# Kernel optimization log

Measured on AMD Instinct MI355X. Metric: run time of the kernel, lower is better.

The kernel has to match this reference:

```python
import jax, jax.numpy as jnp
import numpy as np

BF16_MIN = -3.3895313892515355e+38  # torch.finfo(torch.bfloat16).min
B, S, D = 2, 2048, 2048
H, KVH = 32, 8
HD = D // H  # 64


def setup_inputs() -> dict:
    key = jax.random.key(0)
    ks = jax.random.split(key, 7)
    scale = 0.02
    x = jax.random.normal(ks[0], (B, S, D), dtype=jnp.float32)
    # rotary tables as in llama2.c: theta = 10000^{-2i/hd}
    inv_freq = 1.0 / (10000.0 ** (np.arange(0, HD, 2, dtype=np.float32) / HD))
    t = np.arange(S, dtype=np.float32)
    freqs = np.outer(t, inv_freq)  # (S, HD//2)
    freqs_cos = jnp.asarray(np.cos(freqs))
    freqs_sin = jnp.asarray(np.sin(freqs))
    wq = jax.random.normal(ks[1], (H * HD, D), dtype=jnp.float32) * scale
    wk = jax.random.normal(ks[2], (KVH * HD, D), dtype=jnp.float32) * scale
    wv = jax.random.normal(ks[3], (KVH * HD, D), dtype=jnp.float32) * scale
    wo = jax.random.normal(ks[4], (D, H * HD), dtype=jnp.float32) * scale
    attn_mask = jnp.ones((B, S), dtype=jnp.int32)
    return {"x": x, "freqs_cos": freqs_cos, "freqs_sin": freqs_sin,
            "wq": wq, "wk": wk, "wv": wv, "wo": wo, "attn_mask": attn_mask}


def _rope(x, cos, sin):
    # x: (b, s, h, hd) -> split into interleaved real/imag pairs
    b, s, h, hd = x.shape
    xr = x[..., 0::2]
    xi = x[..., 1::2]
    cos = cos[None, :, None, :]  # (1, s, 1, hd//2)
    sin = sin[None, :, None, :]
    out_r = xr * cos - xi * sin
    out_i = xr * sin + xi * cos
    return jnp.stack([out_r, out_i], axis=-1).reshape(b, s, h, hd)


def reference(x, freqs_cos, freqs_sin, wq, wk, wv, wo, attn_mask):
    b, s, d = x.shape
    n_rep = H // KVH
    xq = jnp.einsum('bsd,ed->bse', x, wq).reshape(b, s, H, HD)
    xk = jnp.einsum('bsd,ed->bse', x, wk).reshape(b, s, KVH, HD)
    xv = jnp.einsum('bsd,ed->bse', x, wv).reshape(b, s, KVH, HD)
    xq = _rope(xq, freqs_cos, freqs_sin)
    xk = _rope(xk, freqs_cos, freqs_sin)
    # GQA repeat_kv: (b, s, kvh, hd) -> (b, s, kvh*n_rep, hd)
    xk = jnp.repeat(xk, n_rep, axis=2)
    xv = jnp.repeat(xv, n_rep, axis=2)
    # (b, h, s, hd)
    xq = xq.transpose(0, 2, 1, 3)
    xk = xk.transpose(0, 2, 1, 3)
    xv = xv.transpose(0, 2, 1, 3)
    causal = jnp.triu(jnp.full((s, s), BF16_MIN, dtype=x.dtype), k=1)[None, None]
    pad = jnp.where(attn_mask[:, None, :] == 0, BF16_MIN, 0.0).astype(x.dtype)  # (b,1,s) -> broadcast over query
    combined = causal + pad[:, None, :, :]  # (b,1,s,s)
    scores = jnp.einsum('bhqd,bhkd->bhqk', xq, xk) / np.sqrt(HD).astype(x.dtype)
    scores = jax.nn.softmax(scores + combined, axis=-1)
    out = jnp.einsum('bhqk,bhkd->bhqd', scores, xv)
    out = out.transpose(0, 2, 1, 3).reshape(b, s, H * HD)
    return jnp.einsum('bse,de->bsd', out, wo)
```

## Files before the change

### kernel.cpp

```cpp
#include <hip/hip_runtime.h>

typedef unsigned short u16;
typedef unsigned int u32;
typedef __attribute__((ext_vector_type(8))) short bf16x8;
typedef __attribute__((ext_vector_type(4))) float f32x4;

#define S_LEN 2048
#define QKV_N 3072
#define CEXP 0.18033688011f
#define M32C 5.77078016f

__device__ __forceinline__ u16 f2bf(float f) {
  u32 u = __builtin_bit_cast(u32, f);
  u32 r = (u + 0x7FFFu + ((u >> 16) & 1u)) >> 16;
  return (u16)r;
}
__device__ __forceinline__ u32 cvtpk(float lo, float hi) {
  u32 r;
  asm("v_cvt_pk_bf16_f32 %0, %1, %2" : "=v"(r) : "v"(lo), "v"(hi));
  return r;
}
__device__ __forceinline__ void gload16(const void* g, void* l) {
  __builtin_amdgcn_global_load_lds(
      (const __attribute__((address_space(1))) u32*)g,
      (__attribute__((address_space(3))) u32*)l, 16, 0, 0);
}

__global__ void cast_all(const float* __restrict__ x, const float* __restrict__ wq,
                         const float* __restrict__ wk, const float* __restrict__ wv,
                         const float* __restrict__ wo, u16* __restrict__ xb,
                         u16* __restrict__ wqkvb, u16* __restrict__ wob) {
  int i = blockIdx.x * 256 + threadIdx.x;
  const float* s;
  u16* d;
  int so, dofs;
  if (i < 2097152) {
    s = x; d = xb; so = i; dofs = i;
  } else if (i < 3145728) {
    s = wq; d = wqkvb; so = i - 2097152; dofs = so;
  } else if (i < 3407872) {
    s = wk; d = wqkvb; so = i - 3145728; dofs = so + 1048576;
  } else if (i < 3670016) {
    s = wv; d = wqkvb; so = i - 3407872; dofs = so + 1310720;
  } else {
    s = wo; d = wob; so = i - 3670016; dofs = so;
  }
  float4 v = ((const float4*)s)[so];
  ((uint2*)d)[dofs] = make_uint2(cvtpk(v.x, v.y), cvtpk(v.z, v.w));
}

template <int BM, int BN, int WM, int WN, int OUT_BF16, int ROPE>
__global__ __launch_bounds__(512, 2) void gemm_bt2(const u16* __restrict__ A,
                                                   const u16* __restrict__ B,
                                                   void* __restrict__ Cv,
                                                   int K, int ldc, int nbx,
                                                   const float* __restrict__ fc,
                                                   const float* __restrict__ fs,
                                                   u16* __restrict__ vt) {
  constexpr int MR = BM / WM / 16;
  constexpr int NR = BN / WN / 16;
  constexpr int MR2 = MR / 2, NR2 = NR / 2;
  constexpr int AR = BM / 64, BR = BN / 64;
  __shared__ u16 As0[BM * 64], As1[BM * 64];
  __shared__ u16 Bs0[BN * 64], Bs1[BN * 64];

  const int tid = threadIdx.x;
  const int lane = tid & 63, w = tid >> 6;
  const int wm = w / WN, wn = w % WN;
  const int g = lane >> 4, r16 = lane & 15;
  const int swz = r16 & 7;

  const int nwg = gridDim.x;
  const int q = nwg >> 3, r = nwg & 7;
  const int xcd = blockIdx.x & 7, off = blockIdx.x >> 3;
  const int wg = (xcd < r ? xcd * (q + 1) : r * (q + 1) + (xcd - r) * q) + off;
  const int m0 = (wg / nbx) * BM, n0 = (wg % nbx) * BN;

  const int rowi = tid >> 3;
  const int scol = ((tid & 7) ^ (rowi & 7)) * 8;
  const u16* Ag0 = A + (size_t)(m0 + rowi) * K + scol;
  const u16* Bg0 = B + (size_t)(n0 + rowi) * K + scol;

  f32x4 acc[MR][NR];
#pragma unroll
  for (int mi = 0; mi < MR; ++mi)
#pragma unroll
    for (int ni = 0; ni < NR; ++ni) acc[mi][ni] = f32x4{0.f, 0.f, 0.f, 0.f};

  auto stage = [&](int kb, u16* Ad, u16* Bd) {
#pragma unroll
    for (int rr = 0; rr < AR; ++rr)
      gload16(Ag0 + (size_t)rr * 64 * K + kb, Ad + rr * 4096 + tid * 8);
#pragma unroll
    for (int rr = 0; rr < BR; ++rr)
      gload16(Bg0 + (size_t)rr * 64 * K + kb, Bd + rr * 4096 + tid * 8);
  };

  auto compute = [&](const u16* Asrc, const u16* Bsrc) {
    bf16x8 ac[MR2][2], bc[NR][2];
    const u16* Aw = Asrc + (wm * MR * 16 + r16) * 64;
    const u16* Bw = Bsrc + (wn * NR * 16 + r16) * 64;
#pragma unroll
    for (int mi = 0; mi < MR2; ++mi)
#pragma unroll
      for (int kk = 0; kk < 2; ++kk)
        ac[mi][kk] = *(const bf16x8*)(Aw + mi * 1024 + ((kk * 4 + g) ^ swz) * 8);
#pragma unroll
    for (int ni = 0; ni < NR2; ++ni)
#pragma unroll
      for (int kk = 0; kk < 2; ++kk)
        bc[ni][kk] = *(const bf16x8*)(Bw + ni * 1024 + ((kk * 4 + g) ^ swz) * 8);
    __builtin_amdgcn_s_setprio(1);
#pragma unroll
    for (int mi = 0; mi < MR2; ++mi)
#pragma unroll
      for (int ni = 0; ni < NR2; ++ni)
#pragma unroll
        for (int kk = 0; kk < 2; ++kk)
          acc[mi][ni] = __builtin_amdgcn_mfma_f32_16x16x32_bf16(
              ac[mi][kk], bc[ni][kk], acc[mi][ni], 0, 0, 0);
    __builtin_amdgcn_s_setprio(0);
#pragma unroll
    for (int ni = NR2; ni < NR; ++ni)
#pragma unroll
      for (int kk = 0; kk < 2; ++kk)
        bc[ni][kk] = *(const bf16x8*)(Bw + ni * 1024 + ((kk * 4 + g) ^ swz) * 8);
    __builtin_amdgcn_s_setprio(1);
#pragma unroll
    for (int mi = 0; mi < MR2; ++mi)
#pragma unroll
      for (int ni = NR2; ni < NR; ++ni)
#pragma unroll
        for (int kk = 0; kk < 2; ++kk)
          acc[mi][ni] = __builtin_amdgcn_mfma_f32_16x16x32_bf16(
              ac[mi][kk], bc[ni][kk], acc[mi][ni], 0, 0, 0);
    __builtin_amdgcn_s_setprio(0);
#pragma unroll
    for (int mi = 0; mi < MR2; ++mi)
#pragma unroll
      for (int kk = 0; kk < 2; ++kk)
        ac[mi][kk] =
            *(const bf16x8*)(Aw + (MR2 + mi) * 1024 + ((kk * 4 + g) ^ swz) * 8);
    __builtin_amdgcn_s_setprio(1);
#pragma unroll
    for (int mi = 0; mi < MR2; ++mi)
#pragma unroll
      for (int ni = NR2; ni < NR; ++ni)
#pragma unroll
        for (int kk = 0; kk < 2; ++kk)
          acc[MR2 + mi][ni] = __builtin_amdgcn_mfma_f32_16x16x32_bf16(
              ac[mi][kk], bc[ni][kk], acc[MR2 + mi][ni], 0, 0, 0);
    __builtin_amdgcn_s_setprio(0);
    __builtin_amdgcn_s_setprio(1);
#pragma unroll
    for (int mi = 0; mi < MR2; ++mi)
#pragma unroll
      for (int ni = 0; ni < NR2; ++ni)
#pragma unroll
        for (int kk = 0; kk < 2; ++kk)
          acc[MR2 + mi][ni] = __builtin_amdgcn_mfma_f32_16x16x32_bf16(
              ac[mi][kk], bc[ni][kk], acc[MR2 + mi][ni], 0, 0, 0);
    __builtin_amdgcn_s_setprio(0);
  };

  const int NT = K >> 6;
  stage(0, As0, Bs0);
  __syncthreads();
  for (int t = 0; t < NT; t += 2) {
    if (t + 1 < NT) stage((t + 1) * 64, As1, Bs1);
    compute(As0, Bs0);
    __syncthreads();
    if (t + 2 < NT) stage((t + 2) * 64, As0, Bs0);
    compute(As1, Bs1);
    __syncthreads();
  }

  if (ROPE && n0 >= 2560) {
#pragma unroll
    for (int mi = 0; mi < MR; ++mi)
#pragma unroll
      for (int ni = 0; ni < NR; ++ni) {
        int row = m0 + wm * MR * 16 + mi * 16 + g * 4;
        int col = n0 + wn * NR * 16 + ni * 16 + r16;
        int kv = (col - 2560) >> 6;
        int d = (col - 2560) & 63;
        int b_ = row >> 11, s0 = row & 2047;
        *(uint2*)&vt[(size_t)((b_ * 8 + kv) * 64 + d) * 2048 + s0] =
            make_uint2(cvtpk(acc[mi][ni][0], acc[mi][ni][1]),
                       cvtpk(acc[mi][ni][2], acc[mi][ni][3]));
      }
    return;
  }

#pragma unroll
  for (int mi = 0; mi < MR; ++mi)
#pragma unroll
    for (int ni = 0; ni < NR; ++ni) {
      int row = m0 + wm * MR * 16 + mi * 16 + g * 4;
      int col = n0 + wn * NR * 16 + ni * 16 + r16;
#pragma unroll
      for (int j = 0; j < 4; ++j) {
        float v = acc[mi][ni][j];
        if (ROPE) {
          float pv = __shfl_xor(v, 1);
          int s = (row + j) & (S_LEN - 1);
          int fi = (col >> 1) & 31;
          float c = fc[s * 32 + fi], sn = fs[s * 32 + fi];
          v = fmaf(pv, (r16 & 1) ? sn : -sn, v * c);
        }
        if (OUT_BF16)
          ((u16*)Cv)[(size_t)(row + j) * ldc + col] = f2bf(v);
        else
          ((float*)Cv)[(size_t)(row + j) * ldc + col] = v;
      }
    }
}

__global__ __launch_bounds__(256, 3) void attn_fwd(const u16* __restrict__ qkv,
                                                   const u16* __restrict__ vt,
                                                   u16* __restrict__ aout) {
  __shared__ u16 Ks[2][64 * 64];
  __shared__ u16 Vs[2][64 * 64];
  __shared__ u16 Ps[4][16 * 64];

  const int bh = blockIdx.x;
  const int y = blockIdx.y;
  const int qt = (y < 4) ? (15 - y) : (y < 8) ? (y - 4) : (y < 12) ? y : (19 - y);
  const int b = bh >> 5, h = bh & 31, kvh = h >> 2;
  const int tid = threadIdx.x;
  const int w = tid >> 6, lane = tid & 63;
  const int g = lane >> 4, r16 = lane & 15;
  const int q0w = qt * 128 + w * 32;

  const u16* kbase = qkv + (size_t)b * S_LEN * QKV_N + 2048 + kvh * 64;
  const u16* vbase = vt + (size_t)(b * 8 + kvh) * 64 * S_LEN;

  const int srow = lane >> 3;
  const int scol = ((lane & 7) * 8) ^ (srow * 8);
  const int swz = (r16 & 7) * 8;

  bf16x8 qf[2][2];
#pragma unroll
  for (int qs = 0; qs < 2; ++qs) {
    const u16* qrow =
        qkv + (size_t)(b * S_LEN + q0w + qs * 16 + r16) * QKV_N + h * 64;
#pragma unroll
    for (int dh = 0; dh < 2; ++dh)
      qf[qs][dh] = *(const bf16x8*)(qrow + dh * 32 + g * 8);
  }

  f32x4 oacc[2][4];
#pragma unroll
  for (int qs = 0; qs < 2; ++qs)
#pragma unroll
    for (int dt = 0; dt < 4; ++dt) oacc[qs][dt] = f32x4{0.f, 0.f, 0.f, 0.f};
  float lsum[2] = {0.f, 0.f};

  const int nt = qt * 2 + 2;
  const int ntw = ((q0w + 31) >> 6) + 1;

#pragma unroll
  for (int c2 = 0; c2 < 2; ++c2) {
    int c = w * 2 + c2;
    gload16(kbase + (size_t)(c * 8 + srow) * QKV_N + scol, &Ks[0][c * 512]);
    gload16(vbase + (size_t)(c * 8 + srow) * 2048 + scol, &Vs[0][c * 512]);
  }
  __syncthreads();

  int cur = 0;
  for (int t = 0; t < nt; ++t) {
    if (t + 1 < nt) {
      int kk0 = (t + 1) * 64;
#pragma unroll
      for (int c2 = 0; c2 < 2; ++c2) {
        int c = w * 2 + c2;
        gload16(kbase + (size_t)(kk0 + c * 8 + srow) * QKV_N + scol,
                &Ks[cur ^ 1][c * 512]);
        gload16(vbase + (size_t)(c * 8 + srow) * 2048 + kk0 + scol,
                &Vs[cur ^ 1][c * 512]);
      }
    }
    if (t < ntw) {
      const int k0 = t * 64;
      bf16x8 kf[4][2];
#pragma unroll
      for (int ks = 0; ks < 4; ++ks)
#pragma unroll
        for (int dh = 0; dh < 2; ++dh)
          kf[ks][dh] = *(const bf16x8*)&Ks[cur][(ks * 16 + r16) * 64 +
                                               ((dh * 32 + g * 8) ^ swz)];
      bf16x8 vfc[2][4];
#pragma unroll
      for (int ks2 = 0; ks2 < 2; ++ks2)
#pragma unroll
        for (int dt = 0; dt < 4; ++dt)
          vfc[ks2][dt] = *(const bf16x8*)&Vs[cur][(dt * 16 + r16) * 64 +
                                                  ((ks2 * 32 + g * 8) ^ swz)];
      const bool needmask = (k0 + 63 > q0w);
#pragma unroll
      for (int qs = 0; qs < 2; ++qs) {
        f32x4 st[4];
        __builtin_amdgcn_s_setprio(1);
#pragma unroll
        for (int ks = 0; ks < 4; ++ks) {
          f32x4 a = f32x4{0.f, 0.f, 0.f, 0.f};
          a = __builtin_amdgcn_mfma_f32_16x16x32_bf16(kf[ks][0], qf[qs][0], a, 0, 0, 0);
          a = __builtin_amdgcn_mfma_f32_16x16x32_bf16(kf[ks][1], qf[qs][1], a, 0, 0, 0);
          st[ks] = a;
        }
        __builtin_amdgcn_s_setprio(0);
        const int qg = q0w + qs * 16 + r16;
        if (needmask) {
#pragma unroll
          for (int ks = 0; ks < 4; ++ks)
#pragma unroll
            for (int j = 0; j < 4; ++j)
              if (k0 + ks * 16 + g * 4 + j > qg) st[ks][j] = -__builtin_inff();
        }
        float ps = 0.f;
#pragma unroll
        for (int ks = 0; ks < 4; ++ks) {
          float p0 = exp2f(fmaf(st[ks][0], CEXP, -M32C));
          float p1 = exp2f(fmaf(st[ks][1], CEXP, -M32C));
          float p2 = exp2f(fmaf(st[ks][2], CEXP, -M32C));
          float p3 = exp2f(fmaf(st[ks][3], CEXP, -M32C));
          ps += (p0 + p1) + (p2 + p3);
          *(uint2*)&Ps[w][r16 * 64 + ((ks * 16 + g * 4) ^ swz)] =
              make_uint2(cvtpk(p0, p1), cvtpk(p2, p3));
        }
        lsum[qs] += ps;
        __builtin_amdgcn_s_setprio(1);
#pragma unroll
        for (int ks2 = 0; ks2 < 2; ++ks2) {
          bf16x8 pf =
              *(const bf16x8*)&Ps[w][r16 * 64 + ((ks2 * 32 + g * 8) ^ swz)];
#pragma unroll
          for (int dt = 0; dt < 4; ++dt)
            oacc[qs][dt] = __builtin_amdgcn_mfma_f32_16x16x32_bf16(
                pf, vfc[ks2][dt], oacc[qs][dt], 0, 0, 0);
        }
        __builtin_amdgcn_s_setprio(0);
      }
    }
    __syncthreads();
    cur ^= 1;
  }

#pragma unroll
  for (int qs = 0; qs < 2; ++qs) {
    float l = lsum[qs];
    l += __shfl_xor(l, 16);
    l += __shfl_xor(l, 32);
    float inv = 1.f / l;
    float iv[4];
#pragma unroll
    for (int j = 0; j < 4; ++j) iv[j] = __shfl(inv, g * 4 + j);
#pragma unroll
    for (int dt = 0; dt < 4; ++dt)
#pragma unroll
      for (int j = 0; j < 4; ++j) {
        size_t o = (size_t)(b * S_LEN + q0w + qs * 16 + g * 4 + j) * 2048 +
                   h * 64 + dt * 16 + r16;
        aout[o] = f2bf(oacc[qs][dt][j] * iv[j]);
      }
  }
}

extern "C" void kernel_launch(void* const* d_in, const int* in_sizes, int n_in,
                              void* d_out, int out_size, void* d_ws,
                              size_t ws_size, hipStream_t stream) {
  const float* x = (const float*)d_in[0];
  const float* fc = (const float*)d_in[1];
  const float* fs = (const float*)d_in[2];
  const float* wq = (const float*)d_in[3];
  const float* wk = (const float*)d_in[4];
  const float* wv = (const float*)d_in[5];
  const float* wo = (const float*)d_in[6];
  float* out = (float*)d_out;

  char* ws = (char*)d_ws;
  u16* xb = (u16*)(ws);
  u16* wqkvb = (u16*)(ws + 16777216);
  u16* wob = (u16*)(ws + 29360128);
  u16* qkvb = (u16*)(ws + 37748736);
  u16* vtb = (u16*)(ws + 62914560);
  u16* aoutb = (u16*)(ws + 67108864);

  cast_all<<<18432, 256, 0, stream>>>(x, wq, wk, wv, wo, xb, wqkvb, wob);

  gemm_bt2<128, 128, 2, 4, 1, 1><<<768, 512, 0, stream>>>(
      xb, wqkvb, qkvb, 2048, 3072, 24, fc, fs, vtb);
  attn_fwd<<<dim3(64, 16), 256, 0, stream>>>(qkvb, vtb, aoutb);
  gemm_bt2<128, 128, 2, 4, 0, 0><<<512, 512, 0, stream>>>(
      aoutb, wob, out, 2048, 2048, 16, nullptr, nullptr, nullptr);
}
```

Before: 171.0 us.

## Halve attention query tile to 64 rows, doubling grid and simplifying masking

Each attention block now handles 64 query rows (16 per wave) instead of 128, and the grid doubles to 32 query tiles per head, launched heaviest-first. The per-wave skip of fully masked KV tiles is gone, and masking is applied only on the last (diagonal) tile. This aims for better load balance and occupancy through more, smaller blocks with fewer registers. The cost is that K/V tiles are loaded from global memory twice as often relative to the query work.

```diff
diff --git a/kernel.cpp b/kernel.cpp
--- a/kernel.cpp
+++ b/kernel.cpp
@@ -224,13 +224,12 @@
   __shared__ u16 Ps[4][16 * 64];
 
   const int bh = blockIdx.x;
-  const int y = blockIdx.y;
-  const int qt = (y < 4) ? (15 - y) : (y < 8) ? (y - 4) : (y < 12) ? y : (19 - y);
+  const int qt = 31 - (int)blockIdx.y;
   const int b = bh >> 5, h = bh & 31, kvh = h >> 2;
   const int tid = threadIdx.x;
   const int w = tid >> 6, lane = tid & 63;
   const int g = lane >> 4, r16 = lane & 15;
-  const int q0w = qt * 128 + w * 32;
+  const int q0w = qt * 64 + w * 16;
 
   const u16* kbase = qkv + (size_t)b * S_LEN * QKV_N + 2048 + kvh * 64;
   const u16* vbase = vt + (size_t)(b * 8 + kvh) * 64 * S_LEN;
@@ -239,25 +238,20 @@
   const int scol = ((lane & 7) * 8) ^ (srow * 8);
   const int swz = (r16 & 7) * 8;
 
-  bf16x8 qf[2][2];
-#pragma unroll
-  for (int qs = 0; qs < 2; ++qs) {
-    const u16* qrow =
-        qkv + (size_t)(b * S_LEN + q0w + qs * 16 + r16) * QKV_N + h * 64;
+  bf16x8 qf[2];
+  {
+    const u16* qrow = qkv + (size_t)(b * S_LEN + q0w + r16) * QKV_N + h * 64;
 #pragma unroll
     for (int dh = 0; dh < 2; ++dh)
-      qf[qs][dh] = *(const bf16x8*)(qrow + dh * 32 + g * 8);
-  }
-
-  f32x4 oacc[2][4];
-#pragma unroll
-  for (int qs = 0; qs < 2; ++qs)
-#pragma unroll
-    for (int dt = 0; dt < 4; ++dt) oacc[qs][dt] = f32x4{0.f, 0.f, 0.f, 0.f};
-  float lsum[2] = {0.f, 0.f};
-
-  const int nt = qt * 2 + 2;
-  const int ntw = ((q0w + 31) >> 6) + 1;
+      qf[dh] = *(const bf16x8*)(qrow + dh * 32 + g * 8);
+  }
+
+  f32x4 oacc[4];
+#pragma unroll
+  for (int dt = 0; dt < 4; ++dt) oacc[dt] = f32x4{0.f, 0.f, 0.f, 0.f};
+  float lsum = 0.f;
+
+  const int nt = qt + 1;
 
 #pragma unroll
   for (int c2 = 0; c2 < 2; ++c2) {
@@ -280,7 +274,7 @@
                 &Vs[cur ^ 1][c * 512]);
       }
     }
-    if (t < ntw) {
+    {
       const int k0 = t * 64;
       bf16x8 kf[4][2];
 #pragma unroll
@@ -296,74 +290,66 @@
         for (int dt = 0; dt < 4; ++dt)
           vfc[ks2][dt] = *(const bf16x8*)&Vs[cur][(dt * 16 + r16) * 64 +
                                                   ((ks2 * 32 + g * 8) ^ swz)];
-      const bool needmask = (k0 + 63 > q0w);
-#pragma unroll
-      for (int qs = 0; qs < 2; ++qs) {
-        f32x4 st[4];
-        __builtin_amdgcn_s_setprio(1);
-#pragma unroll
-        for (int ks = 0; ks < 4; ++ks) {
-          f32x4 a = f32x4{0.f, 0.f, 0.f, 0.f};
-          a = __builtin_amdgcn_mfma_f32_16x16x32_bf16(kf[ks][0], qf[qs][0], a, 0, 0, 0);
-          a = __builtin_amdgcn_mfma_f32_16x16x32_bf16(kf[ks][1], qf[qs][1], a, 0, 0, 0);
-          st[ks] = a;
-        }
-        __builtin_amdgcn_s_setprio(0);
-        const int qg = q0w + qs * 16 + r16;
-        if (needmask) {
-#pragma unroll
-          for (int ks = 0; ks < 4; ++ks)
-#pragma unroll
-            for (int j = 0; j < 4; ++j)
-              if (k0 + ks * 16 + g * 4 + j > qg) st[ks][j] = -__builtin_inff();
-        }
-        float ps = 0.f;
-#pragma unroll
-        for (int ks = 0; ks < 4; ++ks) {
-          float p0 = exp2f(fmaf(st[ks][0], CEXP, -M32C));
-          float p1 = exp2f(fmaf(st[ks][1], CEXP, -M32C));
-          float p2 = exp2f(fmaf(st[ks][2], CEXP, -M32C));
-          float p3 = exp2f(fmaf(st[ks][3], CEXP, -M32C));
-          ps += (p0 + p1) + (p2 + p3);
-          *(uint2*)&Ps[w][r16 * 64 + ((ks * 16 + g * 4) ^ swz)] =
-              make_uint2(cvtpk(p0, p1), cvtpk(p2, p3));
-        }
-        lsum[qs] += ps;
-        __builtin_amdgcn_s_setprio(1);
-#pragma unroll
-        for (int ks2 = 0; ks2 < 2; ++ks2) {
-          bf16x8 pf =
-              *(const bf16x8*)&Ps[w][r16 * 64 + ((ks2 * 32 + g * 8) ^ swz)];
-#pragma unroll
-          for (int dt = 0; dt < 4; ++dt)
-            oacc[qs][dt] = __builtin_amdgcn_mfma_f32_16x16x32_bf16(
-                pf, vfc[ks2][dt], oacc[qs][dt], 0, 0, 0);
-        }
-        __builtin_amdgcn_s_setprio(0);
-      }
+      f32x4 st[4];
+      __builtin_amdgcn_s_setprio(1);
+#pragma unroll
+      for (int ks = 0; ks < 4; ++ks) {
+        f32x4 a = f32x4{0.f, 0.f, 0.f, 0.f};
+        a = __builtin_amdgcn_mfma_f32_16x16x32_bf16(kf[ks][0], qf[0], a, 0, 0, 0);
+        a = __builtin_amdgcn_mfma_f32_16x16x32_bf16(kf[ks][1], qf[1], a, 0, 0, 0);
+        st[ks] = a;
+      }
+      __builtin_amdgcn_s_setprio(0);
+      if (t == nt - 1) {
+        const int qg = q0w + r16;
+#pragma unroll
+        for (int ks = 0; ks < 4; ++ks)
+#pragma unroll
+          for (int j = 0; j < 4; ++j)
+            if (k0 + ks * 16 + g * 4 + j > qg) st[ks][j] = -__builtin_inff();
+      }
+      float ps = 0.f;
+#pragma unroll
+      for (int ks = 0; ks < 4; ++ks) {
+        float p0 = exp2f(fmaf(st[ks][0], CEXP, -M32C));
+        float p1 = exp2f(fmaf(st[ks][1], CEXP, -M32C));
+        float p2 = exp2f(fmaf(st[ks][2], CEXP, -M32C));
+        float p3 = exp2f(fmaf(st[ks][3], CEXP, -M32C));
+        ps += (p0 + p1) + (p2 + p3);
+        *(uint2*)&Ps[w][r16 * 64 + ((ks * 16 + g * 4) ^ swz)] =
+            make_uint2(cvtpk(p0, p1), cvtpk(p2, p3));
+      }
+      lsum += ps;
+      __builtin_amdgcn_s_setprio(1);
+#pragma unroll
+      for (int ks2 = 0; ks2 < 2; ++ks2) {
+        bf16x8 pf = *(const bf16x8*)&Ps[w][r16 * 64 + ((ks2 * 32 + g * 8) ^ swz)];
+#pragma unroll
+        for (int dt = 0; dt < 4; ++dt)
+          oacc[dt] = __builtin_amdgcn_mfma_f32_16x16x32_bf16(
+              pf, vfc[ks2][dt], oacc[dt], 0, 0, 0);
+      }
+      __builtin_amdgcn_s_setprio(0);
     }
     __syncthreads();
     cur ^= 1;
   }
 
-#pragma unroll
-  for (int qs = 0; qs < 2; ++qs) {
-    float l = lsum[qs];
-    l += __shfl_xor(l, 16);
-    l += __shfl_xor(l, 32);
-    float inv = 1.f / l;
-    float iv[4];
-#pragma unroll
-    for (int j = 0; j < 4; ++j) iv[j] = __shfl(inv, g * 4 + j);
-#pragma unroll
-    for (int dt = 0; dt < 4; ++dt)
-#pragma unroll
-      for (int j = 0; j < 4; ++j) {
-        size_t o = (size_t)(b * S_LEN + q0w + qs * 16 + g * 4 + j) * 2048 +
-                   h * 64 + dt * 16 + r16;
-        aout[o] = f2bf(oacc[qs][dt][j] * iv[j]);
-      }
-  }
+  float l = lsum;
+  l += __shfl_xor(l, 16);
+  l += __shfl_xor(l, 32);
+  float inv = 1.f / l;
+  float iv[4];
+#pragma unroll
+  for (int j = 0; j < 4; ++j) iv[j] = __shfl(inv, g * 4 + j);
+#pragma unroll
+  for (int dt = 0; dt < 4; ++dt)
+#pragma unroll
+    for (int j = 0; j < 4; ++j) {
+      size_t o = (size_t)(b * S_LEN + q0w + g * 4 + j) * 2048 + h * 64 +
+                 dt * 16 + r16;
+      aout[o] = f2bf(oacc[dt][j] * iv[j]);
+    }
 }
 
 extern "C" void kernel_launch(void* const* d_in, const int* in_sizes, int n_in,
@@ -390,7 +376,7 @@
 
   gemm_bt2<128, 128, 2, 4, 1, 1><<<768, 512, 0, stream>>>(
       xb, wqkvb, qkvb, 2048, 3072, 24, fc, fs, vtb);
-  attn_fwd<<<dim3(64, 16), 256, 0, stream>>>(qkvb, vtb, aoutb);
+  attn_fwd<<<dim3(64, 32), 256, 0, stream>>>(qkvb, vtb, aoutb);
   gemm_bt2<128, 128, 2, 4, 0, 0><<<512, 512, 0, stream>>>(
       aoutb, wob, out, 2048, 2048, 16, nullptr, nullptr, nullptr);
 }
```

New measurement: 173.4 us. No clear change (+1.4%).
